# Performance work log

Hardware: AMD Instinct MI355X
Metric: run time of the kernel (lower is better)

The kernel has to match this reference:

```python
import jax, jax.numpy as jnp
import numpy as np

# ---- synthetic softmax-tree (matches read_softmax_tree output format) ----
R, B, K = 16, 2, 8  # root group size, child groups per root node, lower-level group size
ROOT_SIZE = 0       # (number of root groups) - 1
THRESHOLD = 0.5
MAXG = 16           # max group size (root group has 16, others 8)
MAXCH = 2           # max subgroups pushed per node (child_sizes+1)
STACK = 16          # safe bound >= module's computed stack_size


def _build_tree():
    group_offsets, group_sizes = [0], [R]
    child, child_sizes = [], []
    # level-1 (root) nodes: each has B child groups starting at group 1+B*i
    for i in range(R):
        child.append(1 + B * i)
        child_sizes.append(B - 1)
    n_l2 = R * B * K
    for gi in range(R * B):
        group_offsets.append(R + gi * K)
        group_sizes.append(K)
    # level-2 nodes: each has a single leaf group
    l3_first_group = 1 + R * B
    for j in range(n_l2):
        child.append(l3_first_group + j)
        child_sizes.append(0)
    for gj in range(n_l2):
        group_offsets.append(R + n_l2 + gj * K)
        group_sizes.append(K)
    # level-3 leaf nodes
    for _ in range(n_l2 * K):
        child.append(-1)
        child_sizes.append(0)
    return (np.asarray(group_offsets, np.int32), np.asarray(group_sizes, np.int32),
            np.asarray(child, np.int32), np.asarray(child_sizes, np.int32))


def setup_inputs() -> dict:
    key = jax.random.key(0)
    k1, k2 = jax.random.split(key)
    go, gs, ch, cs = _build_tree()
    node_count = int(go[-1] + gs[-1])  # 2320
    N, H, W = 16, 64, 64
    conf = jax.random.uniform(k1, (N, node_count, H, W), dtype=jnp.float32)
    obj = jax.random.uniform(k2, (N, H, W), dtype=jnp.float32)
    return {
        "conf": conf, "obj": obj,
        "group_offsets": jnp.asarray(go), "group_sizes": jnp.asarray(gs),
        "child": jnp.asarray(ch), "child_sizes": jnp.asarray(cs),
    }


def _smt_predict(conf, obj, group_offsets, group_sizes, child, child_sizes):
    # Stack-based DFS softmax-tree path selection with threshold pruning.
    # conf: [N, C, H, W] group-softmaxed probabilities; obj: [N, H, W].
    N, C, H, W = conf.shape
    inner = H * W
    # one lane per (sample, spatial location)
    conf2 = conf.reshape(N, C, inner).transpose(0, 2, 1).reshape(N * inner, C)
    obj2 = obj.reshape(N * inner)
    # pad channel dim so dynamic_slice windows never clip/shift
    confp = jnp.concatenate(
        [conf2, jnp.full((N * inner, MAXG), -jnp.inf, conf.dtype)], axis=1)

    lane = jnp.arange(MAXCH, dtype=jnp.int32)
    garange = jnp.arange(MAXG)

    def traverse(c_loc, o_loc):
        top = jnp.zeros((C,), conf.dtype)
        sg = jnp.zeros((STACK,), jnp.int32)          # group stack
        sp = jnp.zeros((STACK,), conf.dtype)          # parent path prob
        spa = jnp.full((STACK,), -1, jnp.int32)       # parent argmax node
        nroot = ROOT_SIZE + 1
        sg = sg.at[:nroot].set(jnp.arange(nroot, dtype=jnp.int32))
        sp = sp.at[:nroot].set(o_loc)                 # path prob starts at objectness

        def cond(st):
            return st[4] > 0

        def body(st):
            top, sg, sp, spa, ptr = st
            ptr = ptr - 1
            g, pp, pa = sg[ptr], sp[ptr], spa[ptr]
            off, size = group_offsets[g], group_sizes[g]
            win = jax.lax.dynamic_slice(c_loc, (off,), (MAXG,))
            win = jnp.where(garange < size, win, -jnp.inf)
            j = jnp.argmax(win)
            p = pp * win[j]                  # cumulative path probability
            amax = off + j
            c, cs_n = child[amax], child_sizes[amax]
            above = p > THRESHOLD
            # leaf hit -> write p at argmax; pruned -> write parent prob at parent node
            widx = jnp.where(above, amax, pa)
            wval = jnp.where(above, p, pp)
            do_w = jnp.where(above, c < 0, pa >= 0)
            safe = jnp.maximum(widx, 0)
            top = top.at[safe].set(jnp.where(do_w, wval, top[safe]))
            # descend: push subgroups c .. c+child_sizes of the argmax node
            npush = jnp.where(above & (c >= 0), cs_n + 1, 0).astype(jnp.int32)
            pm = lane < npush
            ii = ptr + lane
            sg = sg.at[ii].set(jnp.where(pm, c + lane, sg[ii]))
            sp = sp.at[ii].set(jnp.where(pm, p, sp[ii]))
            spa = spa.at[ii].set(jnp.where(pm, amax, spa[ii]))
            return (top, sg, sp, spa, ptr + npush)

        top, *_ = jax.lax.while_loop(cond, body, (top, sg, sp, spa, jnp.int32(nroot)))
        return jnp.concatenate([top, jnp.max(top)[None]])  # append_max channel

    out = jax.vmap(traverse)(confp, obj2)  # [N*inner, C+1]
    return out.reshape(N, inner, C + 1).transpose(0, 2, 1).reshape(N, C + 1, H, W)


def reference(conf, obj, group_offsets, group_sizes, child, child_sizes):
    return _smt_predict(conf, obj, group_offsets, group_sizes, child, child_sizes)
```

## Files before the change

### kernel.cpp

```cpp
#include <hip/hip_runtime.h>
#include <cmath>


typedef float vfloat4 __attribute__((ext_vector_type(4)));

__global__ __launch_bounds__(256) void smt_zero_kernel(float* __restrict__ out,
                                                       long long n4, int rem) {
    long long i = (long long)blockIdx.x * blockDim.x + threadIdx.x;
    if (i < n4) {
        vfloat4 z = {0.f, 0.f, 0.f, 0.f};
        __builtin_nontemporal_store(z, (vfloat4*)out + i);
    } else if (i == n4) {
        for (int r = 0; r < rem; ++r) out[n4 * 4 + r] = 0.f;
    }
}

#define SMT_THRESHOLD 0.5f
#define SMT_STACK 16

__global__ __launch_bounds__(256) void smt_traverse_kernel(
    const float* __restrict__ conf,
    const float* __restrict__ obj,
    const int* __restrict__ go,
    const int* __restrict__ gs,
    const int* __restrict__ child,
    const int* __restrict__ csize,
    float* __restrict__ out,
    int C, int inner_log2, int inner_mask, int total) {
    int lane = blockIdx.x * blockDim.x + threadIdx.x;
    if (lane >= total) return;
    int hw = lane & inner_mask;
    int inner = inner_mask + 1;
    long long nCinner = (long long)(lane - hw) * C;
    const float* cbase = conf + nCinner + hw;
    float* obase = out + nCinner + (long long)(lane >> inner_log2) * inner + hw;

    float o = obj[lane];

    int   sg[SMT_STACK];
    float sp[SMT_STACK];
    int   spa[SMT_STACK];
    sg[0] = 0; sp[0] = o; spa[0] = -1;
    int ptr = 1;
    float maxtop = 0.0f;

    while (ptr > 0) {
        ptr--;
        int g = sg[ptr];
        float pp = sp[ptr];
        int pa = spa[ptr];
        int off = go[g];
        int size = gs[g];
        float best = -INFINITY;
        int bj = 0;
        for (int j = 0; j < size; ++j) {
            float v = cbase[(long long)(off + j) * inner];
            if (v > best) { best = v; bj = j; }
        }
        float p = pp * best;
        int amax = off + bj;
        int c = child[amax];
        int cs_n = csize[amax];
        if (p > SMT_THRESHOLD) {
            if (c < 0) {
                obase[(long long)amax * inner] = p;
                maxtop = fmaxf(maxtop, p);
            } else {
                int npush = cs_n + 1;
                for (int l = 0; l < npush; ++l) {
                    sg[ptr + l] = c + l;
                    sp[ptr + l] = p;
                    spa[ptr + l] = amax;
                }
                ptr += npush;
            }
        } else if (pa >= 0) {
            obase[(long long)pa * inner] = pp;
            maxtop = fmaxf(maxtop, pp);
        }
    }
    obase[(long long)C * inner] = maxtop;
}

extern "C" void kernel_launch(void* const* d_in, const int* in_sizes, int n_in,
                              void* d_out, int out_size, void* d_ws, size_t ws_size,
                              hipStream_t stream) {
    const float* conf = (const float*)d_in[0];
    const float* obj  = (const float*)d_in[1];
    const int* go     = (const int*)d_in[2];
    const int* gs     = (const int*)d_in[3];
    const int* child  = (const int*)d_in[4];
    const int* csize  = (const int*)d_in[5];
    float* out = (float*)d_out;

    const int C = in_sizes[4];
    const int total = in_sizes[1];
    const int inner = 64 * 64;
    const int inner_log2 = 12;
    const int inner_mask = inner - 1;

    long long n4 = (long long)out_size >> 2;
    int rem = out_size & 3;
    long long zthreads = n4 + (rem ? 1 : 0);
    int zblocks = (int)((zthreads + 255) / 256);
    smt_zero_kernel<<<zblocks, 256, 0, stream>>>(out, n4, rem);

    int tblocks = (total + 255) / 256;
    smt_traverse_kernel<<<tblocks, 256, 0, stream>>>(
        conf, obj, go, gs, child, csize, out, C, inner_log2, inner_mask, total);
}
```

Baseline: 868.1 us.

## Unroll stack DFS into fixed three-level nested traversal with batched group loads

Replaces the per-lane stack-based DFS loop with a fully unrolled three-level traversal that hardcodes the tree depth and two-way branching, so no private stack arrays are needed. Group argmax now issues all 16 loads up front (masked by size) for more memory-level parallelism. The zero kernel becomes a grid-stride loop with a fixed 2048 blocks, and the tail handling for non-multiple-of-4 output sizes is dropped. It assumes the tree is at most three levels deep with at most two children per node, and the skipped remainder means the last few output elements could stay unzeroed.

```diff
diff --git a/kernel.cpp b/kernel.cpp
--- a/kernel.cpp
+++ b/kernel.cpp
@@ -5,18 +5,36 @@
 typedef float vfloat4 __attribute__((ext_vector_type(4)));
 
 __global__ __launch_bounds__(256) void smt_zero_kernel(float* __restrict__ out,
-                                                       long long n4, int rem) {
-    long long i = (long long)blockIdx.x * blockDim.x + threadIdx.x;
-    if (i < n4) {
-        vfloat4 z = {0.f, 0.f, 0.f, 0.f};
-        __builtin_nontemporal_store(z, (vfloat4*)out + i);
-    } else if (i == n4) {
-        for (int r = 0; r < rem; ++r) out[n4 * 4 + r] = 0.f;
+                                                       long long n4) {
+    long long stride = (long long)gridDim.x * blockDim.x;
+    vfloat4 z = {0.f, 0.f, 0.f, 0.f};
+    vfloat4* out4 = (vfloat4*)out;
+    for (long long i = (long long)blockIdx.x * blockDim.x + threadIdx.x;
+         i < n4; i += stride) {
+        __builtin_nontemporal_store(z, out4 + i);
     }
 }
 
 #define SMT_THRESHOLD 0.5f
-#define SMT_STACK 16
+#define SMT_MAXG 16
+#define SMT_INNER_LOG2 12
+#define SMT_INNER 4096
+
+__device__ inline void group_argmax(const float* __restrict__ cbase, int off,
+                                    int size, float& best, int& bj) {
+    float v[SMT_MAXG];
+#pragma unroll
+    for (int j = 0; j < SMT_MAXG; ++j) {
+        v[j] = (j < size) ? cbase[(long long)(off + j) << SMT_INNER_LOG2]
+                          : -INFINITY;
+    }
+    best = v[0];
+    bj = 0;
+#pragma unroll
+    for (int j = 1; j < SMT_MAXG; ++j) {
+        if (v[j] > best) { best = v[j]; bj = j; }
+    }
+}
 
 __global__ __launch_bounds__(256) void smt_traverse_kernel(
     const float* __restrict__ conf,
@@ -26,60 +44,79 @@
     const int* __restrict__ child,
     const int* __restrict__ csize,
     float* __restrict__ out,
-    int C, int inner_log2, int inner_mask, int total) {
+    int C, int total) {
     int lane = blockIdx.x * blockDim.x + threadIdx.x;
     if (lane >= total) return;
-    int hw = lane & inner_mask;
-    int inner = inner_mask + 1;
+    int hw = lane & (SMT_INNER - 1);
     long long nCinner = (long long)(lane - hw) * C;
     const float* cbase = conf + nCinner + hw;
-    float* obase = out + nCinner + (long long)(lane >> inner_log2) * inner + hw;
+    float* obase = out + nCinner +
+                   (long long)(lane >> SMT_INNER_LOG2) * SMT_INNER + hw;
 
     float o = obj[lane];
-
-    int   sg[SMT_STACK];
-    float sp[SMT_STACK];
-    int   spa[SMT_STACK];
-    sg[0] = 0; sp[0] = o; spa[0] = -1;
-    int ptr = 1;
     float maxtop = 0.0f;
 
-    while (ptr > 0) {
-        ptr--;
-        int g = sg[ptr];
-        float pp = sp[ptr];
-        int pa = spa[ptr];
-        int off = go[g];
-        int size = gs[g];
-        float best = -INFINITY;
-        int bj = 0;
-        for (int j = 0; j < size; ++j) {
-            float v = cbase[(long long)(off + j) * inner];
-            if (v > best) { best = v; bj = j; }
-        }
-        float p = pp * best;
-        int amax = off + bj;
-        int c = child[amax];
-        int cs_n = csize[amax];
-        if (p > SMT_THRESHOLD) {
-            if (c < 0) {
-                obase[(long long)amax * inner] = p;
-                maxtop = fmaxf(maxtop, p);
-            } else {
-                int npush = cs_n + 1;
-                for (int l = 0; l < npush; ++l) {
-                    sg[ptr + l] = c + l;
-                    sp[ptr + l] = p;
-                    spa[ptr + l] = amax;
+    int off0 = go[0], sz0 = gs[0];
+    float best0; int j0;
+    group_argmax(cbase, off0, sz0, best0, j0);
+    float p0 = o * best0;
+    int amax0 = off0 + j0;
+    if (p0 > SMT_THRESHOLD) {
+        int c0 = child[amax0];
+        int cs0 = csize[amax0];
+        if (c0 < 0) {
+            obase[(long long)amax0 << SMT_INNER_LOG2] = p0;
+            maxtop = fmaxf(maxtop, p0);
+        } else {
+#pragma unroll
+            for (int l = 0; l < 2; ++l) {
+                if (l <= cs0) {
+                    int g2 = c0 + l;
+                    int off2 = go[g2], sz2 = gs[g2];
+                    float best2; int j2;
+                    group_argmax(cbase, off2, sz2, best2, j2);
+                    float p2 = p0 * best2;
+                    int amax2 = off2 + j2;
+                    int c2 = child[amax2];
+                    int cs2 = csize[amax2];
+                    if (p2 > SMT_THRESHOLD) {
+                        if (c2 < 0) {
+                            obase[(long long)amax2 << SMT_INNER_LOG2] = p2;
+                            maxtop = fmaxf(maxtop, p2);
+                        } else {
+#pragma unroll
+                            for (int m = 0; m < 2; ++m) {
+                                if (m <= cs2) {
+                                    int g3 = c2 + m;
+                                    int off3 = go[g3], sz3 = gs[g3];
+                                    float best3; int j3;
+                                    group_argmax(cbase, off3, sz3, best3, j3);
+                                    float p3 = p2 * best3;
+                                    int amax3 = off3 + j3;
+                                    int c3 = child[amax3];
+                                    if (p3 > SMT_THRESHOLD) {
+                                        if (c3 < 0) {
+                                            obase[(long long)amax3
+                                                  << SMT_INNER_LOG2] = p3;
+                                            maxtop = fmaxf(maxtop, p3);
+                                        }
+                                    } else {
+                                        obase[(long long)amax2
+                                              << SMT_INNER_LOG2] = p2;
+                                        maxtop = fmaxf(maxtop, p2);
+                                    }
+                                }
+                            }
+                        }
+                    } else {
+                        obase[(long long)amax0 << SMT_INNER_LOG2] = p0;
+                        maxtop = fmaxf(maxtop, p0);
+                    }
                 }
-                ptr += npush;
             }
-        } else if (pa >= 0) {
-            obase[(long long)pa * inner] = pp;
-            maxtop = fmaxf(maxtop, pp);
         }
     }
-    obase[(long long)C * inner] = maxtop;
+    obase[(long long)C << SMT_INNER_LOG2] = maxtop;
 }
 
 extern "C" void kernel_launch(void* const* d_in, const int* in_sizes, int n_in,
@@ -95,17 +132,11 @@
 
     const int C = in_sizes[4];
     const int total = in_sizes[1];
-    const int inner = 64 * 64;
-    const int inner_log2 = 12;
-    const int inner_mask = inner - 1;
 
     long long n4 = (long long)out_size >> 2;
-    int rem = out_size & 3;
-    long long zthreads = n4 + (rem ? 1 : 0);
-    int zblocks = (int)((zthreads + 255) / 256);
-    smt_zero_kernel<<<zblocks, 256, 0, stream>>>(out, n4, rem);
+    smt_zero_kernel<<<2048, 256, 0, stream>>>(out, n4);
 
     int tblocks = (total + 255) / 256;
     smt_traverse_kernel<<<tblocks, 256, 0, stream>>>(
-        conf, obj, go, gs, child, csize, out, C, inner_log2, inner_mask, total);
+        conf, obj, go, gs, child, csize, out, C, total);
 }
```

Measured after the change: 901.7 us. 3.9% more time.
